# Kernel optimization log

Hardware: AMD Instinct MI355X
Metric: run time of the kernel (lower is better)

## Reference

```python
import jax, jax.numpy as jnp
import numpy as np

B, N, D = 128, 131072, 1

def setup_inputs() -> dict:
    key = jax.random.key(0)
    k1, k2, k3, k4, k5 = jax.random.split(key, 5)
    particles = jax.random.normal(k1, (B, N, D), dtype=jnp.float32)
    particle_weights = jax.random.uniform(k2, (B, N), dtype=jnp.float32)
    observation = jax.random.normal(k3, (B, 1), dtype=jnp.float32)
    noise = jax.random.normal(k4, (B, N, D), dtype=jnp.float32)  # std-normal; scaled by sqrt(10) inside
    uniforms = jax.random.uniform(k5, (B, N), dtype=jnp.float32)
    return {
        "particles": particles,
        "particle_weights": particle_weights,
        "observation": observation,
        "noise": noise,
        "uniforms": uniforms,
        "timestep_number": 3,
    }

def _resample(particles, particle_weights, uniforms):
    # Efficient equivalent of the original O(B*N^2) tile + argmax(cumsum >= u):
    # first index where cumsum >= u  ==  searchsorted(cumsum, u, side='left').
    cum = jnp.cumsum(particle_weights, axis=-1)            # [B, N]
    idx = jax.vmap(lambda c, u: jnp.searchsorted(c, u, side='left'))(cum, uniforms)  # [B, N]
    resampled = jnp.take_along_axis(particles, idx[..., None], axis=1)  # [B, N, D]
    n = particles.shape[1]
    resampled_w = jnp.full(particle_weights.shape, 1.0 / n, dtype=particle_weights.dtype)
    return resampled, resampled_w

def reference(particles, particle_weights, observation, noise, uniforms, timestep_number):
    # Note: the original forward calls resample_particles but then builds the
    # transition from the ORIGINAL particles; resampled values never reach the
    # outputs. We keep the call for fidelity (XLA will DCE it).
    _resampled, _rw = _resample(particles, particle_weights, uniforms)

    # UNGM transition: x/2 + 25*x/(x^2+1) + 8*cos(1.2*t) + N(0, 10)
    mean = particles / 2.0 + 25.0 * (particles / (particles ** 2 + 1.0))
    mean = mean + 8.0 * jnp.cos(1.2 * jnp.float32(timestep_number))
    new_particles = mean + noise * np.float32(np.sqrt(10.0))   # [B, N, 1]

    # Observation likelihood: y ~ N(x^2/20, 1)
    obs_mean = (new_particles ** 2 / 20.0)[..., 0]             # [B, N]
    log_prob = -0.5 * (observation - obs_mean) ** 2 - 0.5 * np.float32(np.log(2.0 * np.pi))
    w = particle_weights * jnp.exp(log_prob)                   # [B, N]
    w = w / jnp.sum(w, axis=1, keepdims=True)
    return new_particles, w
```

## Files before the change

kernel.cpp:

```cpp
#include <hip/hip_runtime.h>
#include <math.h>

#define PF_B 128
#define PF_N 131072
#define TPB 256
#define VPT 4
#define EPT (VPT * 4)
#define EPB (TPB * EPT)
#define BLOCKS_PER_BATCH (PF_N / EPB)

typedef float v4f __attribute__((ext_vector_type(4)));


__device__ __forceinline__ void compute_elem(
    float x, float n, float wt, float c, float ob,
    float& xnew, float& wv)
{
    const float mean = x * 0.5f + 25.0f * (x / (x * x + 1.0f)) + c;
    xnew = mean + n * 3.16227770f;
    const float om = (xnew * xnew) / 20.0f;
    const float d  = ob - om;
    const float lp = -0.5f * d * d + (-0.9189385f);
    wv = wt * __expf(lp);
}

__global__ __launch_bounds__(TPB) void pf_sum(
    const float* __restrict__ particles,
    const float* __restrict__ weights,
    const float* __restrict__ obs,
    const float* __restrict__ noise,
    const int*   __restrict__ tstep,
    float* __restrict__ partials)
{
    const int b     = blockIdx.x / BLOCKS_PER_BATCH;
    const int chunk = blockIdx.x % BLOCKS_PER_BATCH;
    const long base = (long)b * PF_N + (long)chunk * EPB
                    + (long)threadIdx.x * 4;

    const float ob = obs[b];
    const float c  = 8.0f * cosf(1.2f * (float)(*tstep));

    v4f x4[VPT], n4[VPT], wt4[VPT];
    #pragma unroll
    for (int k = 0; k < VPT; ++k)
        x4[k]  = *(const v4f*)(particles + base + (long)k * (TPB * 4));
    #pragma unroll
    for (int k = 0; k < VPT; ++k)
        n4[k]  = *(const v4f*)(noise + base + (long)k * (TPB * 4));
    #pragma unroll
    for (int k = 0; k < VPT; ++k)
        wt4[k] = *(const v4f*)(weights + base + (long)k * (TPB * 4));

    float lsum = 0.0f;
    #pragma unroll
    for (int k = 0; k < VPT; ++k) {
        #pragma unroll
        for (int j = 0; j < 4; ++j) {
            float xn, wv;
            compute_elem(x4[k][j], n4[k][j], wt4[k][j], c, ob, xn, wv);
            lsum += wv;
        }
    }

    #pragma unroll
    for (int off = 32; off > 0; off >>= 1)
        lsum += __shfl_down(lsum, off, 64);

    __shared__ float red[TPB / 64];
    if ((threadIdx.x & 63) == 0) red[threadIdx.x >> 6] = lsum;
    __syncthreads();
    if (threadIdx.x == 0) {
        float s = 0.0f;
        #pragma unroll
        for (int i = 0; i < TPB / 64; ++i) s += red[i];
        partials[blockIdx.x] = s;
    }
}

__global__ __launch_bounds__(TPB) void pf_final(
    const float* __restrict__ particles,
    const float* __restrict__ weights,
    const float* __restrict__ obs,
    const float* __restrict__ noise,
    const int*   __restrict__ tstep,
    const float* __restrict__ partials,
    float* __restrict__ np_out,
    float* __restrict__ w_out)
{
    const int b     = blockIdx.x / BLOCKS_PER_BATCH;
    const int chunk = blockIdx.x % BLOCKS_PER_BATCH;
    const long base = (long)b * PF_N + (long)chunk * EPB
                    + (long)threadIdx.x * 4;

    const float ob = obs[b];
    const float c  = 8.0f * cosf(1.2f * (float)(*tstep));

    const int lane = threadIdx.x & 63;
    float p = partials[b * BLOCKS_PER_BATCH + (lane & (BLOCKS_PER_BATCH - 1))];
    #pragma unroll
    for (int off = BLOCKS_PER_BATCH / 2; off > 0; off >>= 1)
        p += __shfl_xor(p, off, 64);
    const float inv = 1.0f / p;

    v4f x4[VPT], n4[VPT], wt4[VPT];
    #pragma unroll
    for (int k = 0; k < VPT; ++k)
        x4[k]  = *(const v4f*)(particles + base + (long)k * (TPB * 4));
    #pragma unroll
    for (int k = 0; k < VPT; ++k)
        n4[k]  = *(const v4f*)(noise + base + (long)k * (TPB * 4));
    #pragma unroll
    for (int k = 0; k < VPT; ++k)
        wt4[k] = *(const v4f*)(weights + base + (long)k * (TPB * 4));

    #pragma unroll
    for (int k = 0; k < VPT; ++k) {
        v4f xn, wn;
        #pragma unroll
        for (int j = 0; j < 4; ++j) {
            float xnew, wv;
            compute_elem(x4[k][j], n4[k][j], wt4[k][j], c, ob, xnew, wv);
            xn[j] = xnew;
            wn[j] = wv * inv;
        }
        __builtin_nontemporal_store(xn, (v4f*)(np_out + base + (long)k * (TPB * 4)));
        __builtin_nontemporal_store(wn, (v4f*)(w_out  + base + (long)k * (TPB * 4)));
    }
}

extern "C" void kernel_launch(void* const* d_in, const int* in_sizes, int n_in,
                              void* d_out, int out_size, void* d_ws, size_t ws_size,
                              hipStream_t stream) {
    const float* particles = (const float*)d_in[0];
    const float* weights   = (const float*)d_in[1];
    const float* obs       = (const float*)d_in[2];
    const float* noise     = (const float*)d_in[3];
    const int*   tstep     = (const int*)d_in[5];

    float* np_out   = (float*)d_out;
    float* w_out    = (float*)d_out + (long)PF_B * PF_N;
    float* partials = (float*)d_ws;

    const int grid = PF_B * BLOCKS_PER_BATCH;
    pf_sum<<<grid, TPB, 0, stream>>>(particles, weights, obs, noise, tstep,
                                     partials);
    pf_final<<<grid, TPB, 0, stream>>>(particles, weights, obs, noise, tstep,
                                       partials, np_out, w_out);
}
```

Measured before the change: 332.1 us.

## Write unnormalized outputs in first pass and rescale weights in a light second pass

The first kernel now computes and stores the new particles and unnormalized weights while accumulating per-block sums. The second kernel only reads the stored weights back and multiplies them by the inverse batch sum, so it no longer rereads particles, noise and weights or recomputes the transition. This cuts total memory traffic from two full three-input passes to one, plus a read-modify-write of the weight output. The weight store in the first pass is a regular store, so it may stay in cache for the rescale pass.

```diff
diff --git a/kernel.cpp b/kernel.cpp
--- a/kernel.cpp
+++ b/kernel.cpp
@@ -8,6 +8,10 @@
 #define EPT (VPT * 4)
 #define EPB (TPB * EPT)
 #define BLOCKS_PER_BATCH (PF_N / EPB)
+
+#define NORM_BPB 16
+#define NORM_EPB (PF_N / NORM_BPB)
+#define NORM_VPT (NORM_EPB / (TPB * 4))
 
 typedef float v4f __attribute__((ext_vector_type(4)));
 
@@ -24,12 +28,14 @@
     wv = wt * __expf(lp);
 }
 
-__global__ __launch_bounds__(TPB) void pf_sum(
+__global__ __launch_bounds__(TPB) void pf_main(
     const float* __restrict__ particles,
     const float* __restrict__ weights,
     const float* __restrict__ obs,
     const float* __restrict__ noise,
     const int*   __restrict__ tstep,
+    float* __restrict__ np_out,
+    float* __restrict__ w_out,
     float* __restrict__ partials)
 {
     const int b     = blockIdx.x / BLOCKS_PER_BATCH;
@@ -54,12 +60,17 @@
     float lsum = 0.0f;
     #pragma unroll
     for (int k = 0; k < VPT; ++k) {
+        v4f xn, wn;
         #pragma unroll
         for (int j = 0; j < 4; ++j) {
-            float xn, wv;
-            compute_elem(x4[k][j], n4[k][j], wt4[k][j], c, ob, xn, wv);
+            float xnew, wv;
+            compute_elem(x4[k][j], n4[k][j], wt4[k][j], c, ob, xnew, wv);
+            xn[j] = xnew;
+            wn[j] = wv;
             lsum += wv;
         }
+        __builtin_nontemporal_store(xn, (v4f*)(np_out + base + (long)k * (TPB * 4)));
+        *(v4f*)(w_out + base + (long)k * (TPB * 4)) = wn;
     }
 
     #pragma unroll
@@ -77,23 +88,14 @@
     }
 }
 
-__global__ __launch_bounds__(TPB) void pf_final(
-    const float* __restrict__ particles,
-    const float* __restrict__ weights,
-    const float* __restrict__ obs,
-    const float* __restrict__ noise,
-    const int*   __restrict__ tstep,
-    const float* __restrict__ partials,
-    float* __restrict__ np_out,
-    float* __restrict__ w_out)
+__global__ __launch_bounds__(TPB) void pf_norm(
+    float* __restrict__ w_out,
+    const float* __restrict__ partials)
 {
-    const int b     = blockIdx.x / BLOCKS_PER_BATCH;
-    const int chunk = blockIdx.x % BLOCKS_PER_BATCH;
-    const long base = (long)b * PF_N + (long)chunk * EPB
+    const int b     = blockIdx.x / NORM_BPB;
+    const int chunk = blockIdx.x % NORM_BPB;
+    const long base = (long)b * PF_N + (long)chunk * NORM_EPB
                     + (long)threadIdx.x * 4;
-
-    const float ob = obs[b];
-    const float c  = 8.0f * cosf(1.2f * (float)(*tstep));
 
     const int lane = threadIdx.x & 63;
     float p = partials[b * BLOCKS_PER_BATCH + (lane & (BLOCKS_PER_BATCH - 1))];
@@ -102,29 +104,12 @@
         p += __shfl_xor(p, off, 64);
     const float inv = 1.0f / p;
 
-    v4f x4[VPT], n4[VPT], wt4[VPT];
     #pragma unroll
-    for (int k = 0; k < VPT; ++k)
-        x4[k]  = *(const v4f*)(particles + base + (long)k * (TPB * 4));
-    #pragma unroll
-    for (int k = 0; k < VPT; ++k)
-        n4[k]  = *(const v4f*)(noise + base + (long)k * (TPB * 4));
-    #pragma unroll
-    for (int k = 0; k < VPT; ++k)
-        wt4[k] = *(const v4f*)(weights + base + (long)k * (TPB * 4));
-
-    #pragma unroll
-    for (int k = 0; k < VPT; ++k) {
-        v4f xn, wn;
-        #pragma unroll
-        for (int j = 0; j < 4; ++j) {
-            float xnew, wv;
-            compute_elem(x4[k][j], n4[k][j], wt4[k][j], c, ob, xnew, wv);
-            xn[j] = xnew;
-            wn[j] = wv * inv;
-        }
-        __builtin_nontemporal_store(xn, (v4f*)(np_out + base + (long)k * (TPB * 4)));
-        __builtin_nontemporal_store(wn, (v4f*)(w_out  + base + (long)k * (TPB * 4)));
+    for (int k = 0; k < NORM_VPT; ++k) {
+        const long idx = base + (long)k * (TPB * 4);
+        v4f v = *(const v4f*)(w_out + idx);
+        v *= inv;
+        __builtin_nontemporal_store(v, (v4f*)(w_out + idx));
     }
 }
 
@@ -141,9 +126,7 @@
     float* w_out    = (float*)d_out + (long)PF_B * PF_N;
     float* partials = (float*)d_ws;
 
-    const int grid = PF_B * BLOCKS_PER_BATCH;
-    pf_sum<<<grid, TPB, 0, stream>>>(particles, weights, obs, noise, tstep,
-                                     partials);
-    pf_final<<<grid, TPB, 0, stream>>>(particles, weights, obs, noise, tstep,
-                                       partials, np_out, w_out);
+    pf_main<<<PF_B * BLOCKS_PER_BATCH, TPB, 0, stream>>>(
+        particles, weights, obs, noise, tstep, np_out, w_out, partials);
+    pf_norm<<<PF_B * NORM_BPB, TPB, 0, stream>>>(w_out, partials);
 }
```

Measured after the change: 331.4 us. Within noise of the previous version (-0.2%).
